# Kernel optimization log

Hardware: AMD Instinct MI355X
Metric: run time of the kernel (lower is better)

Reference implementation:

```python
import jax, jax.numpy as jnp
import numpy as np

B, L, D, H = 2, 2048, 1024, 16
d = D // H  # head dim = 64


def setup_inputs() -> dict:
    key = jax.random.key(0)
    ks = jax.random.split(key, 6)
    X = jax.random.normal(ks[0], (B, L, D), dtype=jnp.float32)
    scale = 0.02
    Wq = scale * jax.random.normal(ks[1], (D, D), dtype=jnp.float32)
    Wk = scale * jax.random.normal(ks[2], (D, D), dtype=jnp.float32)
    Wv = scale * jax.random.normal(ks[3], (D, D), dtype=jnp.float32)
    Wc = scale * jax.random.normal(ks[4], (D, D), dtype=jnp.float32)
    Ltri = scale * jax.random.normal(ks[5], (H, d, d), dtype=jnp.float32)
    return {"X": X, "Wq": Wq, "Wk": Wk, "Wv": Wv, "Wc": Wc, "Ltri": Ltri}


def reference(X, Wq, Wk, Wv, Wc, Ltri):
    # torch nn.Linear: y = x @ W.T (bias=False); dropout is identity in eval.
    Bsz, Lq, Dm = X.shape
    Q = (X @ Wq.T).reshape(Bsz, Lq, H, d)
    K = (X @ Wk.T).reshape(Bsz, Lq, H, d)
    V = (X @ Wv.T).reshape(Bsz, Lq, H, d)
    # Causal linear attention: cumulative sum of per-position K outer V.
    # W[b,l,h,:,:] = sum_{t<=l} K[b,t,h,:] outer V[b,t,h,:]
    KV = jnp.einsum('blhd,blhe->blhde', K, V)  # [B,L,H,d,d]
    KVc = jnp.cumsum(KV, axis=1)
    Y = jnp.einsum('blhd,blhde->blhe', Q, KVc)  # [B,L,H,d]
    # Learned SPD head-mixing matrix Bm = Lm @ Lm.T with Lm lower-triangular.
    mask = jnp.tril(jnp.ones((1, d, d), dtype=X.dtype))
    Lm = Ltri * mask  # [H,d,d]
    Bm = Lm @ jnp.swapaxes(Lm, -2, -1)  # [H,d,d]
    Y = jnp.einsum('hed,blhd->blhe', Bm, Y)
    Y = Y.reshape(Bsz, Lq, Dm)
    return Y @ Wc.T
```

## Files before the change

kernel.cpp:

```cpp
#include <hip/hip_runtime.h>


#define DEV static __device__ __forceinline__

typedef unsigned short u16;
typedef unsigned long long u64;
typedef __attribute__((ext_vector_type(4))) float f32x4;
typedef __attribute__((ext_vector_type(8))) short bf16x8;

DEV u16 f2bf(float f){
  union { float f; unsigned u; } v; v.f = f;
  unsigned r = v.u + 0x7FFFu + ((v.u >> 16) & 1u);
  return (u16)(r >> 16);
}

DEV void store_val(float* p, float v){ *p = v; }
DEV void store_val(u16* p, float v){ *p = f2bf(v); }

DEV void gload16(const void* g, void* l){
  __builtin_amdgcn_global_load_lds((const __attribute__((address_space(1))) void*)g,
                                   (__attribute__((address_space(3))) void*)l, 16, 0, 0);
}

__global__ __launch_bounds__(256) void prep_kernel(
    const float* __restrict__ X, u16* __restrict__ Xb,
    const float* __restrict__ Wq, u16* __restrict__ Wqb,
    const float* __restrict__ Wk, u16* __restrict__ Wkb,
    const float* __restrict__ Wv, u16* __restrict__ Wvb,
    const float* __restrict__ Wc, u16* __restrict__ Wcb,
    const float* __restrict__ Ltri, u16* __restrict__ Bmb)
{
  const int bx = blockIdx.x, tid = threadIdx.x;
  if(bx < 16){
    __shared__ float Lm[64][65];
    int h = bx;
    const float* src = Ltri + (size_t)h * 4096;
    for(int i = tid; i < 4096; i += 256){
      int e = i >> 6, k = i & 63;
      Lm[e][k] = (k <= e) ? src[i] : 0.f;
    }
    __syncthreads();
    u16* out = Bmb + (size_t)h * 4096;
    for(int i = tid; i < 4096; i += 256){
      int e = i >> 6, dk = i & 63;
      float sum = 0.f;
      int kmax = e < dk ? e : dk;
      for(int k = 0; k <= kmax; k++) sum += Lm[e][k] * Lm[dk][k];
      out[i] = f2bf(sum);
    }
  } else {
    const int n0 = 4194304, n1 = 1048576, n2 = 1048576, n3 = 1048576, n4 = 1048576;
    int total = (n0 + n1 + n2 + n3 + n4) >> 2;
    for(int i = (bx - 16) * 256 + tid; i < total; i += 2048 * 256){
      int e = i << 2;
      const float* s; u16* d;
      if(e < n0){ s = X + e; d = Xb + e; }
      else if(e < n0 + n1){ s = Wq + (e - n0); d = Wqb + (e - n0); }
      else if(e < n0 + n1 + n2){ s = Wk + (e - n0 - n1); d = Wkb + (e - n0 - n1); }
      else if(e < n0 + n1 + n2 + n3){ s = Wv + (e - n0 - n1 - n2); d = Wvb + (e - n0 - n1 - n2); }
      else { s = Wc + (e - n0 - n1 - n2 - n3); d = Wcb + (e - n0 - n1 - n2 - n3); }
      float4 v = *(const float4*)s;
      u64 pk = (u64)f2bf(v.x) | ((u64)f2bf(v.y) << 16) | ((u64)f2bf(v.z) << 32) | ((u64)f2bf(v.w) << 48);
      *(u64*)d = pk;
    }
  }
}

template<typename OutT>
DEV void gemm128_p2(const u16* __restrict__ A, const u16* __restrict__ W,
                    OutT* __restrict__ C, int bx, int by, int N, int K)
{
  __shared__ u16 L[3][8192];
  const int tid = threadIdx.x;
  const int wid = tid >> 6, lane = tid & 63;
  const int wr = wid >> 1, wc = wid & 1;
  const int lr = lane & 15, lq = lane >> 4;
  const u16* Ag = A + (size_t)(bx * 128) * K;
  const u16* Wg = W + (size_t)(by * 128) * K;

  const int p0 = tid >> 3, p1 = 32 + (tid >> 3);
  const int cl0 = (tid & 7) ^ (p0 & 7);
  const int cl1 = (tid & 7) ^ (p1 & 7);
  const int srow0 = 2 * p0 + (cl0 >> 2), skc0 = (cl0 & 3) * 8;
  const int srow1 = 2 * p1 + (cl1 >> 2), skc1 = (cl1 & 3) * 8;

  auto stagef = [&](int kt, int buf){
    gload16(Ag + (size_t)srow0 * K + kt * 32 + skc0, &L[buf][tid * 8]);
    gload16(Ag + (size_t)srow1 * K + kt * 32 + skc1, &L[buf][2048 + tid * 8]);
    gload16(Wg + (size_t)srow0 * K + kt * 32 + skc0, &L[buf][4096 + tid * 8]);
    gload16(Wg + (size_t)srow1 * K + kt * 32 + skc1, &L[buf][6144 + tid * 8]);
  };

  const int nt = K >> 5;
  f32x4 acc[4][4] = {};
  stagef(0, 0);
  stagef(1, 1);
  int cur = 0;
  for(int t = 0; t < nt; t++){
    if(t < nt - 1) asm volatile("s_waitcnt vmcnt(4)" ::: "memory");
    else           asm volatile("s_waitcnt vmcnt(0)" ::: "memory");
    __builtin_amdgcn_s_barrier();
    __builtin_amdgcn_sched_barrier(0);
    if(t + 2 < nt){
      int n2 = cur >= 1 ? cur - 1 : cur + 2;
      stagef(t + 2, n2);
    }
    const u16* Lb = L[cur];
    bf16x8 af[4], bfr[4];
#pragma unroll
    for(int i = 0; i < 4; i++){
      int row = wr * 64 + i * 16 + lr;
      int rh = row >> 1;
      int cph = (lq | ((row & 1) << 2)) ^ (rh & 7);
      af[i] = *(const bf16x8*)&Lb[rh * 64 + cph * 8];
    }
#pragma unroll
    for(int j = 0; j < 4; j++){
      int row = wc * 64 + j * 16 + lr;
      int rh = row >> 1;
      int cph = (lq | ((row & 1) << 2)) ^ (rh & 7);
      bfr[j] = *(const bf16x8*)&Lb[4096 + rh * 64 + cph * 8];
    }
#pragma unroll
    for(int i = 0; i < 4; i++)
#pragma unroll
      for(int j = 0; j < 4; j++)
        acc[i][j] = __builtin_amdgcn_mfma_f32_16x16x32_bf16(af[i], bfr[j], acc[i][j], 0, 0, 0);
    cur = cur == 2 ? 0 : cur + 1;
  }
#pragma unroll
  for(int i = 0; i < 4; i++)
#pragma unroll
    for(int j = 0; j < 4; j++)
#pragma unroll
      for(int r = 0; r < 4; r++){
        int row = bx * 128 + wr * 64 + i * 16 + (lane >> 4) * 4 + r;
        int col = by * 128 + wc * 64 + j * 16 + lr;
        store_val(C + (size_t)row * N + col, acc[i][j][r]);
      }
}

template<typename OutT>
DEV void gemm128_p3(const u16* __restrict__ A, const u16* __restrict__ W,
                    OutT* __restrict__ C, int bx, int by, int N, int K)
{
  __shared__ u16 L[4][8192];
  const int tid = threadIdx.x;
  const int wid = tid >> 6, lane = tid & 63;
  const int wr = wid >> 1, wc = wid & 1;
  const int lr = lane & 15, lq = lane >> 4;
  const u16* Ag = A + (size_t)(bx * 128) * K;
  const u16* Wg = W + (size_t)(by * 128) * K;

  const int p0 = tid >> 3, p1 = 32 + (tid >> 3);
  const int cl0 = (tid & 7) ^ (p0 & 7);
  const int cl1 = (tid & 7) ^ (p1 & 7);
  const int srow0 = 2 * p0 + (cl0 >> 2), skc0 = (cl0 & 3) * 8;
  const int srow1 = 2 * p1 + (cl1 >> 2), skc1 = (cl1 & 3) * 8;

  auto stagef = [&](int kt, int buf){
    gload16(Ag + (size_t)srow0 * K + kt * 32 + skc0, &L[buf][tid * 8]);
    gload16(Ag + (size_t)srow1 * K + kt * 32 + skc1, &L[buf][2048 + tid * 8]);
    gload16(Wg + (size_t)srow0 * K + kt * 32 + skc0, &L[buf][4096 + tid * 8]);
    gload16(Wg + (size_t)srow1 * K + kt * 32 + skc1, &L[buf][6144 + tid * 8]);
  };

  const int nt = K >> 5;
  f32x4 acc[4][4] = {};
  stagef(0, 0);
  stagef(1, 1);
  stagef(2, 2);
  for(int t = 0; t < nt; t++){
    if(t < nt - 2)       asm volatile("s_waitcnt vmcnt(8)" ::: "memory");
    else if(t == nt - 2) asm volatile("s_waitcnt vmcnt(4)" ::: "memory");
    else                 asm volatile("s_waitcnt vmcnt(0)" ::: "memory");
    __builtin_amdgcn_s_barrier();
    __builtin_amdgcn_sched_barrier(0);
    if(t + 3 < nt) stagef(t + 3, (t + 3) & 3);
    const u16* Lb = L[t & 3];
    bf16x8 af[4], bfr[4];
#pragma unroll
    for(int i = 0; i < 4; i++){
      int row = wr * 64 + i * 16 + lr;
      int rh = row >> 1;
      int cph = (lq | ((row & 1) << 2)) ^ (rh & 7);
      af[i] = *(const bf16x8*)&Lb[rh * 64 + cph * 8];
    }
#pragma unroll
    for(int j = 0; j < 4; j++){
      int row = wc * 64 + j * 16 + lr;
      int rh = row >> 1;
      int cph = (lq | ((row & 1) << 2)) ^ (rh & 7);
      bfr[j] = *(const bf16x8*)&Lb[4096 + rh * 64 + cph * 8];
    }
#pragma unroll
    for(int i = 0; i < 4; i++)
#pragma unroll
      for(int j = 0; j < 4; j++)
        acc[i][j] = __builtin_amdgcn_mfma_f32_16x16x32_bf16(af[i], bfr[j], acc[i][j], 0, 0, 0);
  }
#pragma unroll
  for(int i = 0; i < 4; i++)
#pragma unroll
    for(int j = 0; j < 4; j++)
#pragma unroll
      for(int r = 0; r < 4; r++){
        int row = bx * 128 + wr * 64 + i * 16 + (lane >> 4) * 4 + r;
        int col = by * 128 + wc * 64 + j * 16 + lr;
        store_val(C + (size_t)row * N + col, acc[i][j][r]);
      }
}

__global__ __launch_bounds__(256) void qkv_gemm(
    const u16* __restrict__ Xb,
    const u16* __restrict__ Wq, const u16* __restrict__ Wk, const u16* __restrict__ Wv,
    u16* __restrict__ Q, u16* __restrict__ Ko, u16* __restrict__ V)
{
  int sel = blockIdx.y >> 3, byl = blockIdx.y & 7;
  const u16* W = sel == 0 ? Wq : sel == 1 ? Wk : Wv;
  u16* C = sel == 0 ? Q : sel == 1 ? Ko : V;
  gemm128_p2<u16>(Xb, W, C, blockIdx.x, byl, 1024, 1024);
}

__global__ __launch_bounds__(256) void out_gemm(
    const u16* __restrict__ Yb, const u16* __restrict__ Wcpb, float* __restrict__ out)
{
  gemm128_p3<float>(Yb, Wcpb, out, blockIdx.x, blockIdx.y, 1024, 1024);
}

__global__ __launch_bounds__(256) void state_chunk(
    const u16* __restrict__ Kb, const u16* __restrict__ Vb,
    u16* __restrict__ VT, float* __restrict__ Sc)
{
  int bh = blockIdx.x, c = blockIdx.y;
  int b = bh >> 4, h = bh & 15;
  int tid = threadIdx.x;
  __shared__ u16 Kt[128][72];
  __shared__ u16 Vt[128][72];
  __shared__ u16 KtT[64][136];
  __shared__ u16 VtT[64][136];
  int rr = tid >> 3;
  int cc = (tid & 7) * 8;
  const u16* kg = Kb + (size_t)(b * 2048 + c * 128) * 1024 + h * 64;
  const u16* vg = Vb + (size_t)(b * 2048 + c * 128) * 1024 + h * 64;
#pragma unroll
  for(int p = 0; p < 4; p++){
    int row = rr + p * 32;
    *(int4*)&Kt[row][cc] = *(const int4*)(kg + (size_t)row * 1024 + cc);
    *(int4*)&Vt[row][cc] = *(const int4*)(vg + (size_t)row * 1024 + cc);
  }
  __syncthreads();
  int d = tid >> 2, tseg = (tid & 3) * 32;
#pragma unroll
  for(int j = 0; j < 32; j += 8){
    u16 tk[8] __attribute__((aligned(16)));
    u16 tv[8] __attribute__((aligned(16)));
#pragma unroll
    for(int q = 0; q < 8; q++){
      tk[q] = Kt[tseg + j + q][d];
      tv[q] = Vt[tseg + j + q][d];
    }
    *(int4*)&KtT[d][tseg + j] = *(const int4*)tk;
    *(int4*)&VtT[d][tseg + j] = *(const int4*)tv;
  }
  __syncthreads();
  {
    u16* vto = VT + (size_t)bh * 64 * 2048 + (size_t)d * 2048 + c * 128 + tseg;
#pragma unroll
    for(int j = 0; j < 32; j += 8)
      *(int4*)(vto + j) = *(const int4*)&VtT[d][tseg + j];
  }
  int wid = tid >> 6, lane = tid & 63;
  int wr = wid >> 1, wc = wid & 1;
  int lr = lane & 15, lk8 = (lane >> 4) * 8, lq = lane >> 4;
  f32x4 acc[2][2] = {};
#pragma unroll
  for(int ks = 0; ks < 4; ks++){
    bf16x8 a[2], bb[2];
#pragma unroll
    for(int i = 0; i < 2; i++) a[i]  = *(const bf16x8*)&VtT[wr * 32 + i * 16 + lr][ks * 32 + lk8];
#pragma unroll
    for(int j = 0; j < 2; j++) bb[j] = *(const bf16x8*)&KtT[wc * 32 + j * 16 + lr][ks * 32 + lk8];
#pragma unroll
    for(int i = 0; i < 2; i++)
#pragma unroll
      for(int j = 0; j < 2; j++)
        acc[i][j] = __builtin_amdgcn_mfma_f32_16x16x32_bf16(a[i], bb[j], acc[i][j], 0, 0, 0);
  }
  float* out = Sc + ((size_t)bh * 16 + c) * 4096;
#pragma unroll
  for(int i = 0; i < 2; i++)
#pragma unroll
    for(int j = 0; j < 2; j++)
#pragma unroll
      for(int r = 0; r < 4; r++){
        int e = wr * 32 + i * 16 + lq * 4 + r, dk = wc * 32 + j * 16 + lr;
        out[e * 64 + dk] = acc[i][j][r];
      }
}

__global__ __launch_bounds__(256) void prefix_fold(
    const float* __restrict__ Sc, u16* __restrict__ Scb,
    const u16* __restrict__ Wcb, const u16* __restrict__ Bmb, u16* __restrict__ Wcpb)
{
  if(blockIdx.x >= 128){
    int ob = blockIdx.x - 128;
    int rt = ob & 7, h = ob >> 3;
    int wid = threadIdx.x >> 6, lane = threadIdx.x & 63;
    int lr = lane & 15, lk8 = (lane >> 4) * 8, lq = lane >> 4;
    const u16* ab  = Wcb + (size_t)(rt * 128) * 1024 + h * 64;
    const u16* bm  = Bmb + (size_t)h * 4096;
    f32x4 acc[2][4] = {};
#pragma unroll
    for(int i = 0; i < 2; i++){
      int mf = wid * 2 + i;
#pragma unroll
      for(int ks = 0; ks < 2; ks++){
        bf16x8 a = *(const bf16x8*)(ab + (size_t)(mf * 16 + lr) * 1024 + ks * 32 + lk8);
#pragma unroll
        for(int nf = 0; nf < 4; nf++){
          bf16x8 bfr = *(const bf16x8*)(bm + (nf * 16 + lr) * 64 + ks * 32 + lk8);
          acc[i][nf] = __builtin_amdgcn_mfma_f32_16x16x32_bf16(a, bfr, acc[i][nf], 0, 0, 0);
        }
      }
    }
#pragma unroll
    for(int i = 0; i < 2; i++)
#pragma unroll
      for(int nf = 0; nf < 4; nf++)
#pragma unroll
        for(int r = 0; r < 4; r++){
          int row = rt * 128 + (wid * 2 + i) * 16 + lq * 4 + r;
          int col = h * 64 + nf * 16 + lr;
          Wcpb[(size_t)row * 1024 + col] = f2bf(acc[i][nf][r]);
        }
    return;
  }
  int bh = blockIdx.x >> 2, part = blockIdx.x & 3;
  int e4 = part * 256 + threadIdx.x;
  const float4* s = (const float4*)(Sc + (size_t)bh * 65536) + e4;
  u16* d = Scb + (size_t)bh * 65536 + e4 * 4;
  float4 run = {0.f, 0.f, 0.f, 0.f};
  for(int c = 0; c < 16; c++){
    float4 v = s[(size_t)c * 1024];
    u64 pk = (u64)f2bf(run.x) | ((u64)f2bf(run.y) << 16) | ((u64)f2bf(run.z) << 32) | ((u64)f2bf(run.w) << 48);
    *(u64*)(d + (size_t)c * 4096) = pk;
    run.x += v.x; run.y += v.y; run.z += v.z; run.w += v.w;
  }
}

__global__ __launch_bounds__(256) void chunk_attn(
    const u16* __restrict__ Q, const u16* __restrict__ Kmat,
    const u16* __restrict__ VT, const u16* __restrict__ Scb, u16* __restrict__ Y)
{
  int bh = blockIdx.x, c = blockIdx.y;
  int b = bh >> 4, h = bh & 15;
  int t = threadIdx.x, wid = t >> 6, lane = t & 63;
  int lr = lane & 15, lk8 = (lane >> 4) * 8, lq = lane >> 4;
  __shared__ u16 S[128 * 128];
  const u16* qg = Q    + (size_t)(b * 2048 + c * 128) * 1024 + h * 64;
  const u16* kg = Kmat + (size_t)(b * 2048 + c * 128) * 1024 + h * 64;
  const u16* scb = Scb + ((size_t)bh * 16 + c) * 4096;
  const u16* vt  = VT + (size_t)bh * 64 * 2048 + (size_t)c * 128;
  u16* yg = Y + (size_t)(b * 2048 + c * 128) * 1024 + h * 64;

  bf16x8 a[2][2];
#pragma unroll
  for(int mi = 0; mi < 2; mi++){
    int mf = wid + mi * 4;
    int Rm = mf * 16;
    if((mf & 1) == 0){
      int zr = Rm + (lane >> 2), zc = Rm + 16 + (lane & 3) * 4;
      int zoff = ((zr * 128 + zc) * 2) ^ ((zr & 7) << 4);
      *(u64*)((char*)S + zoff) = 0ULL;
    }
#pragma unroll
    for(int ks = 0; ks < 2; ks++) a[mi][ks] = *(const bf16x8*)(qg + (size_t)(Rm + lr) * 1024 + ks * 32 + lk8);
    for(int nf = 0; nf <= mf; nf++){
      f32x4 acc = {};
#pragma unroll
      for(int ks = 0; ks < 2; ks++){
        bf16x8 bb = *(const bf16x8*)(kg + (size_t)(nf * 16 + lr) * 1024 + ks * 32 + lk8);
        acc = __builtin_amdgcn_mfma_f32_16x16x32_bf16(a[mi][ks], bb, acc, 0, 0, 0);
      }
#pragma unroll
      for(int r = 0; r < 4; r++){
        int row = lq * 4 + r, col = lr;
        float v = acc[r];
        if(nf == mf && col > row) v = 0.f;
        int grow = Rm + row, gcol = nf * 16 + col;
        int off = ((grow * 128 + gcol) * 2) ^ ((grow & 7) << 4);
        *(u16*)((char*)S + off) = f2bf(v);
      }
    }
  }
  f32x4 acc2[2][4] = {};
#pragma unroll
  for(int nf = 0; nf < 4; nf++)
#pragma unroll
    for(int ks = 0; ks < 2; ks++){
      bf16x8 bb = *(const bf16x8*)(scb + (nf * 16 + lr) * 64 + ks * 32 + lk8);
#pragma unroll
      for(int mi = 0; mi < 2; mi++)
        acc2[mi][nf] = __builtin_amdgcn_mfma_f32_16x16x32_bf16(a[mi][ks], bb, acc2[mi][nf], 0, 0, 0);
    }
  int ks0 = wid >> 1;
  int row0 = wid * 16 + lr;
  int row1 = (wid + 4) * 16 + lr;
  for(int ks = 0; ks <= ks0 + 2; ks++){
    bf16x8 bb[4];
#pragma unroll
    for(int nf = 0; nf < 4; nf++)
      bb[nf] = *(const bf16x8*)(vt + (size_t)(nf * 16 + lr) * 2048 + ks * 32 + lk8);
    if(ks <= ks0){
      int off = ((row0 * 128 + ks * 32 + lk8) * 2) ^ ((row0 & 7) << 4);
      bf16x8 af = *(const bf16x8*)((char*)S + off);
#pragma unroll
      for(int nf = 0; nf < 4; nf++)
        acc2[0][nf] = __builtin_amdgcn_mfma_f32_16x16x32_bf16(af, bb[nf], acc2[0][nf], 0, 0, 0);
    }
    {
      int off = ((row1 * 128 + ks * 32 + lk8) * 2) ^ ((row1 & 7) << 4);
      bf16x8 af = *(const bf16x8*)((char*)S + off);
#pragma unroll
      for(int nf = 0; nf < 4; nf++)
        acc2[1][nf] = __builtin_amdgcn_mfma_f32_16x16x32_bf16(af, bb[nf], acc2[1][nf], 0, 0, 0);
    }
  }
#pragma unroll
  for(int mi = 0; mi < 2; mi++){
    int Rm = (wid + mi * 4) * 16;
#pragma unroll
    for(int nf = 0; nf < 4; nf++)
#pragma unroll
      for(int r = 0; r < 4; r++){
        int grow = Rm + lq * 4 + r, gcol = nf * 16 + lr;
        yg[(size_t)grow * 1024 + gcol] = f2bf(acc2[mi][nf][r]);
      }
  }
}

extern "C" void kernel_launch(void* const* d_in, const int* in_sizes, int n_in,
                              void* d_out, int out_size, void* d_ws, size_t ws_size,
                              hipStream_t stream)
{
  const float* X    = (const float*)d_in[0];
  const float* Wq   = (const float*)d_in[1];
  const float* Wk   = (const float*)d_in[2];
  const float* Wv   = (const float*)d_in[3];
  const float* Wc   = (const float*)d_in[4];
  const float* Ltri = (const float*)d_in[5];
  float* out = (float*)d_out;

  char* ws = (char*)d_ws;
  size_t off = 0;
  auto carve = [&](size_t bytes) -> char* {
    char* p = ws + off;
    off += (bytes + 255) & ~(size_t)255;
    return p;
  };
  u16* Xb   = (u16*)carve((size_t)4194304 * 2);
  u16* Wqb  = (u16*)carve((size_t)1048576 * 2);
  u16* Wkb  = (u16*)carve((size_t)1048576 * 2);
  u16* Wvb  = (u16*)carve((size_t)1048576 * 2);
  u16* Wcb  = (u16*)carve((size_t)1048576 * 2);
  u16* Wcpb = (u16*)carve((size_t)1048576 * 2);
  u16* Bmb  = (u16*)carve((size_t)65536 * 2);
  u16* Qb   = (u16*)carve((size_t)4194304 * 2);
  u16* Kb   = (u16*)carve((size_t)4194304 * 2);
  u16* Vb   = (u16*)carve((size_t)4194304 * 2);
  u16* VT   = (u16*)carve((size_t)4194304 * 2);
  float* Sc = (float*)carve((size_t)2097152 * 4);
  u16* Scb  = (u16*)carve((size_t)2097152 * 2);
  u16* Yb   = (u16*)carve((size_t)4194304 * 2);
  (void)in_sizes; (void)n_in; (void)out_size; (void)ws_size;

  prep_kernel<<<2064, 256, 0, stream>>>(X, Xb, Wq, Wqb, Wk, Wkb, Wv, Wvb, Wc, Wcb, Ltri, Bmb);
  qkv_gemm<<<dim3(32, 24), 256, 0, stream>>>(Xb, Wqb, Wkb, Wvb, Qb, Kb, Vb);
  state_chunk<<<dim3(32, 16), 256, 0, stream>>>(Kb, Vb, VT, Sc);
  prefix_fold<<<256, 256, 0, stream>>>(Sc, Scb, Wcb, Bmb, Wcpb);
  chunk_attn<<<dim3(32, 16), 256, 0, stream>>>(Qb, Kb, VT, Scb, Yb);
  out_gemm<<<dim3(32, 8), 256, 0, stream>>>(Yb, Wcpb, out);
}
```

Before: 106.3 us.

## Fuse fp32-to-bf16 conversion into QKV GEMM loads and drop prep kernel

Removes the separate prep kernel. The QKV GEMM now reads fp32 X and weights directly into registers, converts them to bf16 and writes them to LDS in a register-staged double buffer, replacing the async global_load_lds triple buffer. The Bm computation and Wc conversion move into the prefix_fold weight-fold blocks. This saves one launch and a full bf16 round-trip of X and the weights through memory. In exchange the GEMM loads twice the bytes per tile, converts on the fly, and loses the direct-to-LDS async pipeline, which may hurt its overlap.

```diff
diff --git a/kernel.cpp b/kernel.cpp
--- a/kernel.cpp
+++ b/kernel.cpp
@@ -22,61 +22,20 @@
                                    (__attribute__((address_space(3))) void*)l, 16, 0, 0);
 }
 
-__global__ __launch_bounds__(256) void prep_kernel(
-    const float* __restrict__ X, u16* __restrict__ Xb,
-    const float* __restrict__ Wq, u16* __restrict__ Wqb,
-    const float* __restrict__ Wk, u16* __restrict__ Wkb,
-    const float* __restrict__ Wv, u16* __restrict__ Wvb,
-    const float* __restrict__ Wc, u16* __restrict__ Wcb,
-    const float* __restrict__ Ltri, u16* __restrict__ Bmb)
-{
-  const int bx = blockIdx.x, tid = threadIdx.x;
-  if(bx < 16){
-    __shared__ float Lm[64][65];
-    int h = bx;
-    const float* src = Ltri + (size_t)h * 4096;
-    for(int i = tid; i < 4096; i += 256){
-      int e = i >> 6, k = i & 63;
-      Lm[e][k] = (k <= e) ? src[i] : 0.f;
-    }
-    __syncthreads();
-    u16* out = Bmb + (size_t)h * 4096;
-    for(int i = tid; i < 4096; i += 256){
-      int e = i >> 6, dk = i & 63;
-      float sum = 0.f;
-      int kmax = e < dk ? e : dk;
-      for(int k = 0; k <= kmax; k++) sum += Lm[e][k] * Lm[dk][k];
-      out[i] = f2bf(sum);
-    }
-  } else {
-    const int n0 = 4194304, n1 = 1048576, n2 = 1048576, n3 = 1048576, n4 = 1048576;
-    int total = (n0 + n1 + n2 + n3 + n4) >> 2;
-    for(int i = (bx - 16) * 256 + tid; i < total; i += 2048 * 256){
-      int e = i << 2;
-      const float* s; u16* d;
-      if(e < n0){ s = X + e; d = Xb + e; }
-      else if(e < n0 + n1){ s = Wq + (e - n0); d = Wqb + (e - n0); }
-      else if(e < n0 + n1 + n2){ s = Wk + (e - n0 - n1); d = Wkb + (e - n0 - n1); }
-      else if(e < n0 + n1 + n2 + n3){ s = Wv + (e - n0 - n1 - n2); d = Wvb + (e - n0 - n1 - n2); }
-      else { s = Wc + (e - n0 - n1 - n2 - n3); d = Wcb + (e - n0 - n1 - n2 - n3); }
-      float4 v = *(const float4*)s;
-      u64 pk = (u64)f2bf(v.x) | ((u64)f2bf(v.y) << 16) | ((u64)f2bf(v.z) << 32) | ((u64)f2bf(v.w) << 48);
-      *(u64*)d = pk;
-    }
-  }
-}
-
-template<typename OutT>
-DEV void gemm128_p2(const u16* __restrict__ A, const u16* __restrict__ W,
-                    OutT* __restrict__ C, int bx, int by, int N, int K)
-{
-  __shared__ u16 L[3][8192];
+__global__ __launch_bounds__(256) void qkv_gemm(
+    const float* __restrict__ X,
+    const float* __restrict__ Wq, const float* __restrict__ Wk, const float* __restrict__ Wv,
+    u16* __restrict__ Q, u16* __restrict__ Ko, u16* __restrict__ V)
+{
+  __shared__ __align__(16) u16 L[2][8192];
+  int sel = blockIdx.y >> 3, byl = blockIdx.y & 7;
+  const float* W = sel == 0 ? Wq : sel == 1 ? Wk : Wv;
+  u16* C = sel == 0 ? Q : sel == 1 ? Ko : V;
+  const int bx = blockIdx.x;
   const int tid = threadIdx.x;
   const int wid = tid >> 6, lane = tid & 63;
   const int wr = wid >> 1, wc = wid & 1;
   const int lr = lane & 15, lq = lane >> 4;
-  const u16* Ag = A + (size_t)(bx * 128) * K;
-  const u16* Wg = W + (size_t)(by * 128) * K;
 
   const int p0 = tid >> 3, p1 = 32 + (tid >> 3);
   const int cl0 = (tid & 7) ^ (p0 & 7);
@@ -84,28 +43,40 @@
   const int srow0 = 2 * p0 + (cl0 >> 2), skc0 = (cl0 & 3) * 8;
   const int srow1 = 2 * p1 + (cl1 >> 2), skc1 = (cl1 & 3) * 8;
 
-  auto stagef = [&](int kt, int buf){
-    gload16(Ag + (size_t)srow0 * K + kt * 32 + skc0, &L[buf][tid * 8]);
-    gload16(Ag + (size_t)srow1 * K + kt * 32 + skc1, &L[buf][2048 + tid * 8]);
-    gload16(Wg + (size_t)srow0 * K + kt * 32 + skc0, &L[buf][4096 + tid * 8]);
-    gload16(Wg + (size_t)srow1 * K + kt * 32 + skc1, &L[buf][6144 + tid * 8]);
+  const float* A0 = X + (size_t)(bx * 128 + srow0) * 1024 + skc0;
+  const float* A1 = X + (size_t)(bx * 128 + srow1) * 1024 + skc1;
+  const float* W0 = W + (size_t)(byl * 128 + srow0) * 1024 + skc0;
+  const float* W1 = W + (size_t)(byl * 128 + srow1) * 1024 + skc1;
+
+  float4 r0, r1, r2, r3, r4, r5, r6, r7;
+  auto issue = [&](int kt){
+    r0 = *(const float4*)(A0 + kt * 32);  r1 = *(const float4*)(A0 + kt * 32 + 4);
+    r2 = *(const float4*)(A1 + kt * 32);  r3 = *(const float4*)(A1 + kt * 32 + 4);
+    r4 = *(const float4*)(W0 + kt * 32);  r5 = *(const float4*)(W0 + kt * 32 + 4);
+    r6 = *(const float4*)(W1 + kt * 32);  r7 = *(const float4*)(W1 + kt * 32 + 4);
   };
-
-  const int nt = K >> 5;
+  auto writebuf = [&](u16* Lb){
+    float4 g[8] = {r0, r1, r2, r3, r4, r5, r6, r7};
+#pragma unroll
+    for(int q = 0; q < 4; q++){
+      u16 h[8] __attribute__((aligned(16)));
+      float4 x0 = g[q * 2], x1 = g[q * 2 + 1];
+      h[0] = f2bf(x0.x); h[1] = f2bf(x0.y); h[2] = f2bf(x0.z); h[3] = f2bf(x0.w);
+      h[4] = f2bf(x1.x); h[5] = f2bf(x1.y); h[6] = f2bf(x1.z); h[7] = f2bf(x1.w);
+      *(int4*)&Lb[q * 2048 + tid * 8] = *(const int4*)h;
+    }
+  };
+
+  const int nt = 32;
   f32x4 acc[4][4] = {};
-  stagef(0, 0);
-  stagef(1, 1);
-  int cur = 0;
+  issue(0);
+  writebuf(L[0]);
+  issue(1);
+  asm volatile("s_waitcnt lgkmcnt(0)" ::: "memory");
+  __builtin_amdgcn_s_barrier();
+
   for(int t = 0; t < nt; t++){
-    if(t < nt - 1) asm volatile("s_waitcnt vmcnt(4)" ::: "memory");
-    else           asm volatile("s_waitcnt vmcnt(0)" ::: "memory");
-    __builtin_amdgcn_s_barrier();
-    __builtin_amdgcn_sched_barrier(0);
-    if(t + 2 < nt){
-      int n2 = cur >= 1 ? cur - 1 : cur + 2;
-      stagef(t + 2, n2);
-    }
-    const u16* Lb = L[cur];
+    const u16* Lb = L[t & 1];
     bf16x8 af[4], bfr[4];
 #pragma unroll
     for(int i = 0; i < 4; i++){
@@ -126,7 +97,13 @@
 #pragma unroll
       for(int j = 0; j < 4; j++)
         acc[i][j] = __builtin_amdgcn_mfma_f32_16x16x32_bf16(af[i], bfr[j], acc[i][j], 0, 0, 0);
-    cur = cur == 2 ? 0 : cur + 1;
+    __builtin_amdgcn_s_barrier();
+    if(t + 1 < nt){
+      writebuf(L[(t + 1) & 1]);
+      if(t + 2 < nt) issue(t + 2);
+      asm volatile("s_waitcnt lgkmcnt(0)" ::: "memory");
+      __builtin_amdgcn_s_barrier();
+    }
   }
 #pragma unroll
   for(int i = 0; i < 4; i++)
@@ -134,23 +111,24 @@
     for(int j = 0; j < 4; j++)
 #pragma unroll
       for(int r = 0; r < 4; r++){
-        int row = bx * 128 + wr * 64 + i * 16 + (lane >> 4) * 4 + r;
-        int col = by * 128 + wc * 64 + j * 16 + lr;
-        store_val(C + (size_t)row * N + col, acc[i][j][r]);
-      }
-}
-
-template<typename OutT>
-DEV void gemm128_p3(const u16* __restrict__ A, const u16* __restrict__ W,
-                    OutT* __restrict__ C, int bx, int by, int N, int K)
+        int row = bx * 128 + wr * 64 + i * 16 + lq * 4 + r;
+        int col = byl * 128 + wc * 64 + j * 16 + lr;
+        C[(size_t)row * 1024 + col] = f2bf(acc[i][j][r]);
+      }
+}
+
+__global__ __launch_bounds__(256) void out_gemm(
+    const u16* __restrict__ Yb, const u16* __restrict__ Wcpb, float* __restrict__ out)
 {
   __shared__ u16 L[4][8192];
+  const int bx = blockIdx.x, by = blockIdx.y;
+  const int K = 1024, N = 1024;
   const int tid = threadIdx.x;
   const int wid = tid >> 6, lane = tid & 63;
   const int wr = wid >> 1, wc = wid & 1;
   const int lr = lane & 15, lq = lane >> 4;
-  const u16* Ag = A + (size_t)(bx * 128) * K;
-  const u16* Wg = W + (size_t)(by * 128) * K;
+  const u16* Ag = Yb + (size_t)(bx * 128) * K;
+  const u16* Wg = Wcpb + (size_t)(by * 128) * K;
 
   const int p0 = tid >> 3, p1 = 32 + (tid >> 3);
   const int cl0 = (tid & 7) ^ (p0 & 7);
@@ -205,27 +183,10 @@
     for(int j = 0; j < 4; j++)
 #pragma unroll
       for(int r = 0; r < 4; r++){
-        int row = bx * 128 + wr * 64 + i * 16 + (lane >> 4) * 4 + r;
+        int row = bx * 128 + wr * 64 + i * 16 + lq * 4 + r;
         int col = by * 128 + wc * 64 + j * 16 + lr;
-        store_val(C + (size_t)row * N + col, acc[i][j][r]);
-      }
-}
-
-__global__ __launch_bounds__(256) void qkv_gemm(
-    const u16* __restrict__ Xb,
-    const u16* __restrict__ Wq, const u16* __restrict__ Wk, const u16* __restrict__ Wv,
-    u16* __restrict__ Q, u16* __restrict__ Ko, u16* __restrict__ V)
-{
-  int sel = blockIdx.y >> 3, byl = blockIdx.y & 7;
-  const u16* W = sel == 0 ? Wq : sel == 1 ? Wk : Wv;
-  u16* C = sel == 0 ? Q : sel == 1 ? Ko : V;
-  gemm128_p2<u16>(Xb, W, C, blockIdx.x, byl, 1024, 1024);
-}
-
-__global__ __launch_bounds__(256) void out_gemm(
-    const u16* __restrict__ Yb, const u16* __restrict__ Wcpb, float* __restrict__ out)
-{
-  gemm128_p3<float>(Yb, Wcpb, out, blockIdx.x, blockIdx.y, 1024, 1024);
+        out[(size_t)row * N + col] = acc[i][j][r];
+      }
 }
 
 __global__ __launch_bounds__(256) void state_chunk(
@@ -301,26 +262,50 @@
 
 __global__ __launch_bounds__(256) void prefix_fold(
     const float* __restrict__ Sc, u16* __restrict__ Scb,
-    const u16* __restrict__ Wcb, const u16* __restrict__ Bmb, u16* __restrict__ Wcpb)
+    const float* __restrict__ Wc, const float* __restrict__ Ltri, u16* __restrict__ Wcpb)
 {
   if(blockIdx.x >= 128){
+    __shared__ float Lm[64][65];
+    __shared__ float Bmf[64][64];
     int ob = blockIdx.x - 128;
     int rt = ob & 7, h = ob >> 3;
-    int wid = threadIdx.x >> 6, lane = threadIdx.x & 63;
+    int tid = threadIdx.x;
+    const float* src = Ltri + (size_t)h * 4096;
+    for(int i = tid; i < 4096; i += 256){
+      int e = i >> 6, k = i & 63;
+      Lm[e][k] = (k <= e) ? src[i] : 0.f;
+    }
+    __syncthreads();
+    for(int i = tid; i < 4096; i += 256){
+      int e = i >> 6, dk = i & 63;
+      float sum = 0.f;
+      int kmax = e < dk ? e : dk;
+      for(int k = 0; k <= kmax; k++) sum += Lm[e][k] * Lm[dk][k];
+      Bmf[e][dk] = sum;
+    }
+    __syncthreads();
+    int wid = tid >> 6, lane = tid & 63;
     int lr = lane & 15, lk8 = (lane >> 4) * 8, lq = lane >> 4;
-    const u16* ab  = Wcb + (size_t)(rt * 128) * 1024 + h * 64;
-    const u16* bm  = Bmb + (size_t)h * 4096;
+    const float* ab = Wc + (size_t)(rt * 128) * 1024 + h * 64;
     f32x4 acc[2][4] = {};
 #pragma unroll
     for(int i = 0; i < 2; i++){
       int mf = wid * 2 + i;
 #pragma unroll
       for(int ks = 0; ks < 2; ks++){
-        bf16x8 a = *(const bf16x8*)(ab + (size_t)(mf * 16 + lr) * 1024 + ks * 32 + lk8);
+        const float* ar = ab + (size_t)(mf * 16 + lr) * 1024 + ks * 32 + lk8;
+        u16 ha[8] __attribute__((aligned(16)));
+#pragma unroll
+        for(int q = 0; q < 8; q++) ha[q] = f2bf(ar[q]);
+        bf16x8 a = *(const bf16x8*)ha;
 #pragma unroll
         for(int nf = 0; nf < 4; nf++){
-          bf16x8 bfr = *(const bf16x8*)(bm + (nf * 16 + lr) * 64 + ks * 32 + lk8);
-          acc[i][nf] = __builtin_amdgcn_mfma_f32_16x16x32_bf16(a, bfr, acc[i][nf], 0, 0, 0);
+          const float* br = &Bmf[nf * 16 + lr][ks * 32 + lk8];
+          u16 hb[8] __attribute__((aligned(16)));
+#pragma unroll
+          for(int q = 0; q < 8; q++) hb[q] = f2bf(br[q]);
+          bf16x8 b = *(const bf16x8*)hb;
+          acc[i][nf] = __builtin_amdgcn_mfma_f32_16x16x32_bf16(a, b, acc[i][nf], 0, 0, 0);
         }
       }
     }
@@ -459,26 +444,19 @@
     off += (bytes + 255) & ~(size_t)255;
     return p;
   };
-  u16* Xb   = (u16*)carve((size_t)4194304 * 2);
-  u16* Wqb  = (u16*)carve((size_t)1048576 * 2);
-  u16* Wkb  = (u16*)carve((size_t)1048576 * 2);
-  u16* Wvb  = (u16*)carve((size_t)1048576 * 2);
-  u16* Wcb  = (u16*)carve((size_t)1048576 * 2);
-  u16* Wcpb = (u16*)carve((size_t)1048576 * 2);
-  u16* Bmb  = (u16*)carve((size_t)65536 * 2);
   u16* Qb   = (u16*)carve((size_t)4194304 * 2);
   u16* Kb   = (u16*)carve((size_t)4194304 * 2);
   u16* Vb   = (u16*)carve((size_t)4194304 * 2);
   u16* VT   = (u16*)carve((size_t)4194304 * 2);
   float* Sc = (float*)carve((size_t)2097152 * 4);
   u16* Scb  = (u16*)carve((size_t)2097152 * 2);
+  u16* Wcpb = (u16*)carve((size_t)1048576 * 2);
   u16* Yb   = (u16*)carve((size_t)4194304 * 2);
   (void)in_sizes; (void)n_in; (void)out_size; (void)ws_size;
 
-  prep_kernel<<<2064, 256, 0, stream>>>(X, Xb, Wq, Wqb, Wk, Wkb, Wv, Wvb, Wc, Wcb, Ltri, Bmb);
-  qkv_gemm<<<dim3(32, 24), 256, 0, stream>>>(Xb, Wqb, Wkb, Wvb, Qb, Kb, Vb);
+  qkv_gemm<<<dim3(32, 24), 256, 0, stream>>>(X, Wq, Wk, Wv, Qb, Kb, Vb);
   state_chunk<<<dim3(32, 16), 256, 0, stream>>>(Kb, Vb, VT, Sc);
-  prefix_fold<<<256, 256, 0, stream>>>(Sc, Scb, Wcb, Bmb, Wcpb);
+  prefix_fold<<<256, 256, 0, stream>>>(Sc, Scb, Wc, Ltri, Wcpb);
   chunk_attn<<<dim3(32, 16), 256, 0, stream>>>(Qb, Kb, VT, Scb, Yb);
   out_gemm<<<dim3(32, 8), 256, 0, stream>>>(Yb, Wcpb, out);
 }
```

New measurement: 120.2 us. 1.13x slower.
